# Optimization experiments

Measured on AMD Instinct MI355X. Metric: run time of the kernel, lower is better.

Reference implementation:

```python
import jax, jax.numpy as jnp
import numpy as np

B, S, D = 4, 2048, 1024
H, HD = 16, 64
WINDOW = 128


def setup_inputs() -> dict:
    key = jax.random.key(0)
    ks = jax.random.split(key, 8)
    scale = 1.0 / np.sqrt(D)
    return {
        "hidden_states": jax.random.normal(ks[0], (B, S, D), dtype=jnp.float32),
        "attention_mask": jnp.zeros((B, 1, 1, S), dtype=jnp.float32),
        "Wq": jax.random.normal(ks[1], (D, D), dtype=jnp.float32) * scale,
        "bq": jnp.zeros((D,), dtype=jnp.float32),
        "Wk": jax.random.normal(ks[2], (D, D), dtype=jnp.float32) * scale,
        "bk": jnp.zeros((D,), dtype=jnp.float32),
        "Wv": jax.random.normal(ks[3], (D, D), dtype=jnp.float32) * scale,
        "bv": jnp.zeros((D,), dtype=jnp.float32),
    }


def _proj(x, W, b):
    # [b t D] -> [b h t d]
    p = x @ W.T + b
    return p.reshape(x.shape[0], x.shape[1], H, HD).transpose(0, 2, 1, 3)


def reference(hidden_states, attention_mask, Wq, bq, Wk, bk, Wv, bv):
    q = _proj(hidden_states, Wq, bq)  # [b h t d]
    k = _proj(hidden_states, Wk, bk)
    v = _proj(hidden_states, Wv, bv)

    scores = jnp.einsum("bhtd,bhsd->bhts", q, k) / np.sqrt(HD)  # [b h t s]
    pos = jnp.arange(S)
    i, j = pos[:, None], pos[None, :]
    # causal (j <= i) AND sliding window (i - j <= w)
    allowed = (j <= i) & ((i - j) <= WINDOW)  # [t s]
    scores = jnp.where(allowed[None, None], scores, -jnp.inf)
    scores = scores + attention_mask  # additive padding mask [b,1,1,s]
    probs = jax.nn.softmax(scores, axis=-1)  # dropout identity in eval
    ctx = jnp.einsum("bhts,bhsd->bhtd", probs, v)
    return ctx.transpose(0, 2, 1, 3).reshape(B, S, D)
```

## Files before the change

kernel.cpp:

```cpp
#include <hip/hip_runtime.h>
#include <cstdint>

#define BDIM 4
#define SEQ 2048
#define DMODEL 1024
#define NH 16
#define HDIM 64

typedef __attribute__((ext_vector_type(8))) short bf16x8;
typedef __attribute__((ext_vector_type(4))) float f32x4;
typedef __attribute__((ext_vector_type(4))) int i32x4;
typedef __attribute__((ext_vector_type(4))) unsigned short u16x4;

#define MFMA16(a, b, c) __builtin_amdgcn_mfma_f32_16x16x32_bf16(a, b, c, 0, 0, 0)

__device__ __forceinline__ unsigned short f2bf(float x) {
    unsigned int u = __float_as_uint(x);
    unsigned int r = (u + 0x7FFFu + ((u >> 16) & 1u)) >> 16;
    return (unsigned short)r;
}

__device__ __forceinline__ void gload16(const void* g, void* l) {
    __builtin_amdgcn_global_load_lds(
        (const __attribute__((address_space(1))) unsigned int*)g,
        (__attribute__((address_space(3))) unsigned int*)l, 16, 0, 0);
}

__global__ __launch_bounds__(256) void k_cvt_x(const float* __restrict__ src,
                                               unsigned short* __restrict__ dst) {
    int i = blockIdx.x * 256 + threadIdx.x;
    float4 v = ((const float4*)src)[i];
    u16x4 o = {f2bf(v.x), f2bf(v.y), f2bf(v.z), f2bf(v.w)};
    ((u16x4*)dst)[i] = o;
}

__global__ __launch_bounds__(256) void k_cvt_w(const float* __restrict__ wq,
                                               const float* __restrict__ wk,
                                               const float* __restrict__ wv,
                                               unsigned short* __restrict__ dst) {
    int i = blockIdx.x * 256 + threadIdx.x;
    int e = i << 2;
    int which = e >> 20;
    int off = e & 0xFFFFF;
    const float* s = which == 0 ? wq : (which == 1 ? wk : wv);
    float4 v = *(const float4*)(s + off);
    u16x4 o = {f2bf(v.x), f2bf(v.y), f2bf(v.z), f2bf(v.w)};
    ((u16x4*)dst)[i] = o;
}

__global__ __launch_bounds__(256) __attribute__((amdgpu_waves_per_eu(4)))
void k_qkv(const unsigned short* __restrict__ X,
           const unsigned short* __restrict__ W,
           const float* __restrict__ bq,
           const float* __restrict__ bk,
           const float* __restrict__ bv,
           unsigned short* __restrict__ Qo,
           unsigned short* __restrict__ Ko,
           unsigned short* __restrict__ Vt) {
    __shared__ unsigned short ldsA[128 * 64];
    __shared__ unsigned short ldsB[128 * 64];
    const int tid = threadIdx.x;
    const int lane = tid & 63, wid = tid >> 6;
    const int wm = wid >> 1, wn = wid & 1;
    const int l15 = lane & 15, g = lane >> 4;
    const int m0 = blockIdx.y * 128, n0 = blockIdx.x * 128;

    f32x4 acc[4][4];
#pragma unroll
    for (int i = 0; i < 4; ++i)
#pragma unroll
        for (int j = 0; j < 4; ++j) acc[i][j] = (f32x4){0.f, 0.f, 0.f, 0.f};

    for (int kt = 0; kt < 16; ++kt) {
        const int k0 = kt << 6;
        __syncthreads();
#pragma unroll
        for (int it = 0; it < 4; ++it) {
            const int c = it * 256 + tid;
            const int row = c >> 3, sl = c & 7;
            const int slx = sl ^ (row & 7);
            gload16(X + (size_t)(m0 + row) * DMODEL + k0 + slx * 8, (char*)ldsA + c * 16);
            gload16(W + (size_t)(n0 + row) * DMODEL + k0 + slx * 8, (char*)ldsB + c * 16);
        }
        __syncthreads();
#pragma unroll
        for (int kk = 0; kk < 2; ++kk) {
            bf16x8 a[4], b[4];
#pragma unroll
            for (int f = 0; f < 4; ++f) {
                const int ra = wm * 64 + f * 16 + l15;
                a[f] = *(const bf16x8*)((const char*)ldsA +
                        ((ra * 128 + kk * 64 + g * 16) ^ ((ra & 7) << 4)));
                const int rb = wn * 64 + f * 16 + l15;
                b[f] = *(const bf16x8*)((const char*)ldsB +
                        ((rb * 128 + kk * 64 + g * 16) ^ ((rb & 7) << 4)));
            }
#pragma unroll
            for (int fm = 0; fm < 4; ++fm)
#pragma unroll
                for (int fn = 0; fn < 4; ++fn) acc[fm][fn] = MFMA16(a[fm], b[fn], acc[fm][fn]);
        }
    }

    const int bb = m0 >> 11;
    const int sbase = (m0 & 2047) + wm * 64 + g * 4;
#pragma unroll
    for (int fn = 0; fn < 4; ++fn) {
        const int col = n0 + wn * 64 + fn * 16 + l15;
        const int proj = col >> 10, rem = col & 1023;
        const int h = rem >> 6, hd = rem & 63;
        const float bias = (proj == 0 ? bq : proj == 1 ? bk : bv)[rem];
        const float scl = (proj == 0) ? 0.125f : 1.0f;
        unsigned short* dstp = (proj == 0 ? Qo : proj == 1 ? Ko : Vt) +
                               (size_t)(bb * NH + h) * (SEQ * HDIM) +
                               (proj == 2 ? (size_t)hd * SEQ : (size_t)hd);
        const int stride = (proj == 2) ? 1 : HDIM;
#pragma unroll
        for (int fm = 0; fm < 4; ++fm) {
            const int s0 = sbase + fm * 16;
#pragma unroll
            for (int r = 0; r < 4; ++r)
                dstp[(size_t)(s0 + r) * stride] = f2bf((acc[fm][fn][r] + bias) * scl);
        }
    }
}

__global__ __launch_bounds__(256) void k_attn(const unsigned short* __restrict__ Qg,
                                              const unsigned short* __restrict__ Kg,
                                              const unsigned short* __restrict__ Vtg,
                                              const float* __restrict__ amask,
                                              float* __restrict__ out) {
    __shared__ unsigned short kl[224 * 64];
    __shared__ unsigned short vl[64 * 224];
    __shared__ unsigned short pl[4 * 16 * 160];
    const int bid0 = blockIdx.x;
    const int bid = (bid0 & 7) * 256 + (bid0 >> 3);
    const int bh = bid >> 5, qb = bid & 31;
    const int b = bh >> 4, h = bh & 15;
    const int q0 = qb << 6;
    const int kstart = q0 - 144;
    const int tid = threadIdx.x, lane = tid & 63, w = tid >> 6;
    const int l15 = lane & 15, g = lane >> 4;

#pragma unroll
    for (int it = 0; it < 7; ++it) {
        const int c = it * 256 + tid;
        {
            const int row = c >> 3, sl = c & 7;
            const int key = kstart + row;
            i32x4 v = {0, 0, 0, 0};
            if ((unsigned)key < (unsigned)SEQ)
                v = *(const i32x4*)(Kg + (size_t)(bh * SEQ + key) * HDIM + sl * 8);
            *(i32x4*)((char*)kl + ((row * 128 + sl * 16) ^ ((row & 7) << 4))) = v;
        }
        {
            const int row = c / 28, sl = c - row * 28;
            const int key0 = kstart + sl * 8;
            i32x4 v = {0, 0, 0, 0};
            if ((unsigned)key0 < (unsigned)SEQ)
                v = *(const i32x4*)(Vtg + (size_t)(bh * HDIM + row) * SEQ + key0);
            *(i32x4*)((char*)vl + ((row * 448 + sl * 16) ^ ((row & 7) << 4))) = v;
        }
    }
    const int iq = q0 + w * 16 + l15;
    const bf16x8 qf0 = *(const bf16x8*)(Qg + (size_t)(bh * SEQ + iq) * HDIM + g * 8);
    const bf16x8 qf1 = *(const bf16x8*)(Qg + (size_t)(bh * SEQ + iq) * HDIM + 32 + g * 8);
    __syncthreads();

    char* pbase = (char*)pl + w * 5120;
    const int swq = (l15 & 7) << 4;
    float s[40];

    __builtin_amdgcn_s_setprio(1);
#pragma unroll
    for (int t = 0; t < 5; ++t) {
        const int tloc = w * 16 + t * 32;
        bf16x8 kf[2][2];
#pragma unroll
        for (int m = 0; m < 2; ++m) {
            const int row = tloc + m * 16 + l15;
            const int swz = (row & 7) << 4;
            kf[m][0] = *(const bf16x8*)((const char*)kl + ((row * 128 + g * 16) ^ swz));
            kf[m][1] = *(const bf16x8*)((const char*)kl + ((row * 128 + 64 + g * 16) ^ swz));
        }
        f32x4 sa0 = {0.f, 0.f, 0.f, 0.f}, sa1 = {0.f, 0.f, 0.f, 0.f};
        sa0 = MFMA16(kf[0][0], qf0, sa0);
        sa0 = MFMA16(kf[0][1], qf1, sa0);
        sa1 = MFMA16(kf[1][0], qf0, sa1);
        sa1 = MFMA16(kf[1][1], qf1, sa1);
#pragma unroll
        for (int f = 0; f < 2; ++f) {
            const int jb = kstart + tloc + f * 16 + g * 4;
            float4 m4 = {0.f, 0.f, 0.f, 0.f};
            if ((unsigned)jb < (unsigned)SEQ) m4 = *(const float4*)(amask + b * SEQ + jb);
            const float mvv[4] = {m4.x, m4.y, m4.z, m4.w};
#pragma unroll
            for (int r = 0; r < 4; ++r) {
                const int jg = jb + r;
                const float sc = (f == 0 ? sa0[r] : sa1[r]) + mvv[r];
                const bool ok = (jg >= 0) && (jg <= iq) && (iq - jg <= 128);
                s[t * 8 + f * 4 + r] = ok ? sc : -3.0e38f;
            }
        }
    }
    __builtin_amdgcn_s_setprio(0);

    float tr[20];
#pragma unroll
    for (int i = 0; i < 20; ++i) tr[i] = fmaxf(s[i], s[i + 20]);
#pragma unroll
    for (int i = 0; i < 10; ++i) tr[i] = fmaxf(tr[i], tr[i + 10]);
#pragma unroll
    for (int i = 0; i < 5; ++i) tr[i] = fmaxf(tr[i], tr[i + 5]);
    float m = fmaxf(fmaxf(tr[0], tr[1]), fmaxf(tr[2], fmaxf(tr[3], tr[4])));
    m = fmaxf(m, __shfl_xor(m, 16));
    m = fmaxf(m, __shfl_xor(m, 32));

    float ls0 = 0.f, ls1 = 0.f, ls2 = 0.f, ls3 = 0.f;
#pragma unroll
    for (int i = 0; i < 40; i += 4) {
        float p0 = exp2f((s[i + 0] - m) * 1.44269504f);
        float p1 = exp2f((s[i + 1] - m) * 1.44269504f);
        float p2 = exp2f((s[i + 2] - m) * 1.44269504f);
        float p3 = exp2f((s[i + 3] - m) * 1.44269504f);
        s[i + 0] = p0; s[i + 1] = p1; s[i + 2] = p2; s[i + 3] = p3;
        ls0 += p0; ls1 += p1; ls2 += p2; ls3 += p3;
    }
    float l = (ls0 + ls1) + (ls2 + ls3);
    l += __shfl_xor(l, 16);
    l += __shfl_xor(l, 32);

#pragma unroll
    for (int t = 0; t < 5; ++t) {
#pragma unroll
        for (int f = 0; f < 2; ++f) {
            u16x4 pu = {f2bf(s[t * 8 + f * 4 + 0]), f2bf(s[t * 8 + f * 4 + 1]),
                        f2bf(s[t * 8 + f * 4 + 2]), f2bf(s[t * 8 + f * 4 + 3])};
            *(u16x4*)(pbase + ((l15 * 320 + t * 64 + f * 32 + g * 8) ^ swq)) = pu;
        }
    }
    asm volatile("s_waitcnt lgkmcnt(0)" ::: "memory");
    __builtin_amdgcn_sched_barrier(0);

    f32x4 acc[4];
#pragma unroll
    for (int i = 0; i < 4; ++i) acc[i] = (f32x4){0.f, 0.f, 0.f, 0.f};
    __builtin_amdgcn_s_setprio(1);
#pragma unroll
    for (int t = 0; t < 5; ++t) {
        const int tloc = w * 16 + t * 32;
        const bf16x8 pf = *(const bf16x8*)(pbase + ((l15 * 320 + t * 64 + g * 16) ^ swq));
#pragma unroll
        for (int fn = 0; fn < 4; ++fn) {
            const int vrow = fn * 16 + l15;
            const bf16x8 vf = *(const bf16x8*)((const char*)vl +
                ((vrow * 448 + tloc * 2 + g * 16) ^ ((vrow & 7) << 4)));
            acc[fn] = MFMA16(pf, vf, acc[fn]);
        }
    }
    __builtin_amdgcn_s_setprio(0);

    float linv[4];
#pragma unroll
    for (int r = 0; r < 4; ++r) linv[r] = 1.0f / __shfl(l, g * 4 + r);
#pragma unroll
    for (int fn = 0; fn < 4; ++fn) {
#pragma unroll
        for (int r = 0; r < 4; ++r) {
            const int qrow = q0 + w * 16 + g * 4 + r;
            out[(size_t)(b * SEQ + qrow) * DMODEL + h * HDIM + fn * 16 + l15] =
                acc[fn][r] * linv[r];
        }
    }
}

extern "C" void kernel_launch(void* const* d_in, const int* in_sizes, int n_in,
                              void* d_out, int out_size, void* d_ws, size_t ws_size,
                              hipStream_t stream) {
    const float* hs = (const float*)d_in[0];
    const float* amask = (const float*)d_in[1];
    const float* wq = (const float*)d_in[2];
    const float* bq = (const float*)d_in[3];
    const float* wk = (const float*)d_in[4];
    const float* bk = (const float*)d_in[5];
    const float* wv = (const float*)d_in[6];
    const float* bv = (const float*)d_in[7];
    float* out = (float*)d_out;

    char* p = (char*)d_ws;
    unsigned short* Xbf = (unsigned short*)p;
    unsigned short* Wbf = (unsigned short*)(p + 16777216);
    unsigned short* Vtb = (unsigned short*)(p + 16777216 + 6291456);
    unsigned short* Qb = Vtb + 8388608;
    unsigned short* Kb = Qb + 8388608;

    k_cvt_x<<<8192, 256, 0, stream>>>(hs, Xbf);
    k_cvt_w<<<3072, 256, 0, stream>>>(wq, wk, wv, Wbf);
    k_qkv<<<dim3(24, 64), 256, 0, stream>>>(Xbf, Wbf, bq, bk, bv, Qb, Kb, Vtb);
    k_attn<<<2048, 256, 0, stream>>>(Qb, Kb, Vtb, amask, out);
}
```

Measured before the change: 138.2 us.

## Rewrite QKV GEMM as 256x256 tile with double-buffered async LDS pipeline

The QKV projection GEMM moves from 128x128 tiles with 256 threads to 256x256 tiles with 512 threads (8 waves, each owning 128x64). LDS is double-buffered in K-halves so global-to-LDS loads for later K steps overlap the MFMA work, with explicit vmcnt waits, barriers and s_setprio. The aim is more data reuse per tile and hidden load latency. The costs are only 384 blocks (fewer than before, with possible wave quantization on the CU count), more accumulator registers, and the loss of the XOR swizzle on LDS, which may bring back bank conflicts.

New measurement: 154.3 us. 11.6% more time.

```diff
diff --git a/kernel.cpp b/kernel.cpp
--- a/kernel.cpp
+++ b/kernel.cpp
@@ -48,7 +48,7 @@
     ((u16x4*)dst)[i] = o;
 }
 
-__global__ __launch_bounds__(256) __attribute__((amdgpu_waves_per_eu(4)))
+__global__ __launch_bounds__(512, 2)
 void k_qkv(const unsigned short* __restrict__ X,
            const unsigned short* __restrict__ W,
            const float* __restrict__ bq,
@@ -57,56 +57,137 @@
            unsigned short* __restrict__ Qo,
            unsigned short* __restrict__ Ko,
            unsigned short* __restrict__ Vt) {
-    __shared__ unsigned short ldsA[128 * 64];
-    __shared__ unsigned short ldsB[128 * 64];
+    __shared__ unsigned short ldsA[2][2][256 * 32];
+    __shared__ unsigned short ldsB[2][2][256 * 32];
     const int tid = threadIdx.x;
     const int lane = tid & 63, wid = tid >> 6;
-    const int wm = wid >> 1, wn = wid & 1;
+    const int wm = wid >> 2, wn = wid & 3;
     const int l15 = lane & 15, g = lane >> 4;
-    const int m0 = blockIdx.y * 128, n0 = blockIdx.x * 128;
-
-    f32x4 acc[4][4];
-#pragma unroll
-    for (int i = 0; i < 4; ++i)
+    const int m0 = blockIdx.y * 256, n0 = blockIdx.x * 256;
+
+#define STAGE_A(c, kk, kt)                                                        \
+    {                                                                             \
+        _Pragma("unroll") for (int i = 0; i < 2; ++i) {                           \
+            const int e = i * 512 + tid;                                          \
+            const int row = e >> 2, cc = e & 3;                                   \
+            gload16(X + (size_t)(m0 + row) * DMODEL + (kt)*64 + (kk)*32 + cc * 8, \
+                    (char*)&ldsA[c][kk][0] + e * 16);                             \
+        }                                                                         \
+    }
+#define STAGE_B(c, kk, kt)                                                        \
+    {                                                                             \
+        _Pragma("unroll") for (int i = 0; i < 2; ++i) {                           \
+            const int e = i * 512 + tid;                                          \
+            const int row = e >> 2, cc = e & 3;                                   \
+            gload16(W + (size_t)(n0 + row) * DMODEL + (kt)*64 + (kk)*32 + cc * 8, \
+                    (char*)&ldsB[c][kk][0] + e * 16);                             \
+        }                                                                         \
+    }
+
+    f32x4 acc[8][4];
+#pragma unroll
+    for (int i = 0; i < 8; ++i)
 #pragma unroll
         for (int j = 0; j < 4; ++j) acc[i][j] = (f32x4){0.f, 0.f, 0.f, 0.f};
 
-    for (int kt = 0; kt < 16; ++kt) {
-        const int k0 = kt << 6;
-        __syncthreads();
-#pragma unroll
-        for (int it = 0; it < 4; ++it) {
-            const int c = it * 256 + tid;
-            const int row = c >> 3, sl = c & 7;
-            const int slx = sl ^ (row & 7);
-            gload16(X + (size_t)(m0 + row) * DMODEL + k0 + slx * 8, (char*)ldsA + c * 16);
-            gload16(W + (size_t)(n0 + row) * DMODEL + k0 + slx * 8, (char*)ldsB + c * 16);
-        }
-        __syncthreads();
-#pragma unroll
-        for (int kk = 0; kk < 2; ++kk) {
-            bf16x8 a[4], b[4];
-#pragma unroll
-            for (int f = 0; f < 4; ++f) {
-                const int ra = wm * 64 + f * 16 + l15;
-                a[f] = *(const bf16x8*)((const char*)ldsA +
-                        ((ra * 128 + kk * 64 + g * 16) ^ ((ra & 7) << 4)));
-                const int rb = wn * 64 + f * 16 + l15;
-                b[f] = *(const bf16x8*)((const char*)ldsB +
-                        ((rb * 128 + kk * 64 + g * 16) ^ ((rb & 7) << 4)));
-            }
-#pragma unroll
-            for (int fm = 0; fm < 4; ++fm)
-#pragma unroll
-                for (int fn = 0; fn < 4; ++fn) acc[fm][fn] = MFMA16(a[fm], b[fn], acc[fm][fn]);
+    STAGE_A(0, 0, 0); STAGE_B(0, 0, 0);
+    STAGE_A(0, 1, 0); STAGE_B(0, 1, 0);
+    STAGE_A(1, 0, 1); STAGE_B(1, 0, 1);
+    asm volatile("s_waitcnt vmcnt(8)" ::: "memory");
+    __builtin_amdgcn_s_barrier();
+
+    const int arow = wm * 128 + l15;
+    const int brow = wn * 64 + l15;
+
+    for (int t = 0; t < 16; ++t) {
+        const int c = t & 1;
+        const char* Ab0 = (const char*)&ldsA[c][0][0];
+        const char* Ab1 = (const char*)&ldsA[c][1][0];
+        const char* Bb0 = (const char*)&ldsB[c][0][0];
+        const char* Bb1 = (const char*)&ldsB[c][1][0];
+
+        {
+            bf16x8 av[8], bv0, bv1;
+#pragma unroll
+            for (int mf = 0; mf < 8; ++mf)
+                av[mf] = *(const bf16x8*)(Ab0 + (arow + mf * 16) * 64 + g * 16);
+            bv0 = *(const bf16x8*)(Bb0 + (brow) * 64 + g * 16);
+            bv1 = *(const bf16x8*)(Bb0 + (brow + 16) * 64 + g * 16);
+            if (t < 15) STAGE_A(c ^ 1, 1, t + 1);
+            __builtin_amdgcn_s_barrier();
+            asm volatile("s_waitcnt lgkmcnt(0)" ::: "memory");
+            __builtin_amdgcn_sched_barrier(0);
+            __builtin_amdgcn_s_setprio(1);
+#pragma unroll
+            for (int mf = 0; mf < 8; ++mf) {
+                acc[mf][0] = MFMA16(av[mf], bv0, acc[mf][0]);
+                acc[mf][1] = MFMA16(av[mf], bv1, acc[mf][1]);
+            }
+            __builtin_amdgcn_s_setprio(0);
+            __builtin_amdgcn_s_barrier();
+
+            bv0 = *(const bf16x8*)(Bb0 + (brow + 32) * 64 + g * 16);
+            bv1 = *(const bf16x8*)(Bb0 + (brow + 48) * 64 + g * 16);
+            if (t < 15) STAGE_B(c ^ 1, 1, t + 1);
+            __builtin_amdgcn_s_barrier();
+            asm volatile("s_waitcnt lgkmcnt(0)" ::: "memory");
+            __builtin_amdgcn_sched_barrier(0);
+            __builtin_amdgcn_s_setprio(1);
+#pragma unroll
+            for (int mf = 0; mf < 8; ++mf) {
+                acc[mf][2] = MFMA16(av[mf], bv0, acc[mf][2]);
+                acc[mf][3] = MFMA16(av[mf], bv1, acc[mf][3]);
+            }
+            __builtin_amdgcn_s_setprio(0);
+            if (t < 15) { asm volatile("s_waitcnt vmcnt(8)" ::: "memory"); }
+            else        { asm volatile("s_waitcnt vmcnt(0)" ::: "memory"); }
+            __builtin_amdgcn_s_barrier();
+        }
+
+        {
+            bf16x8 av[8], bv0, bv1;
+#pragma unroll
+            for (int mf = 0; mf < 8; ++mf)
+                av[mf] = *(const bf16x8*)(Ab1 + (arow + mf * 16) * 64 + g * 16);
+            bv0 = *(const bf16x8*)(Bb1 + (brow) * 64 + g * 16);
+            bv1 = *(const bf16x8*)(Bb1 + (brow + 16) * 64 + g * 16);
+            if (t < 14) STAGE_A(c, 0, t + 2);
+            __builtin_amdgcn_s_barrier();
+            asm volatile("s_waitcnt lgkmcnt(0)" ::: "memory");
+            __builtin_amdgcn_sched_barrier(0);
+            __builtin_amdgcn_s_setprio(1);
+#pragma unroll
+            for (int mf = 0; mf < 8; ++mf) {
+                acc[mf][0] = MFMA16(av[mf], bv0, acc[mf][0]);
+                acc[mf][1] = MFMA16(av[mf], bv1, acc[mf][1]);
+            }
+            __builtin_amdgcn_s_setprio(0);
+            __builtin_amdgcn_s_barrier();
+
+            bv0 = *(const bf16x8*)(Bb1 + (brow + 32) * 64 + g * 16);
+            bv1 = *(const bf16x8*)(Bb1 + (brow + 48) * 64 + g * 16);
+            if (t < 14) STAGE_B(c, 0, t + 2);
+            __builtin_amdgcn_s_barrier();
+            asm volatile("s_waitcnt lgkmcnt(0)" ::: "memory");
+            __builtin_amdgcn_sched_barrier(0);
+            __builtin_amdgcn_s_setprio(1);
+#pragma unroll
+            for (int mf = 0; mf < 8; ++mf) {
+                acc[mf][2] = MFMA16(av[mf], bv0, acc[mf][2]);
+                acc[mf][3] = MFMA16(av[mf], bv1, acc[mf][3]);
+            }
+            __builtin_amdgcn_s_setprio(0);
+            if (t < 14)      { asm volatile("s_waitcnt vmcnt(8)" ::: "memory"); }
+            else if (t == 14){ asm volatile("s_waitcnt vmcnt(4)" ::: "memory"); }
+            __builtin_amdgcn_s_barrier();
         }
     }
 
     const int bb = m0 >> 11;
-    const int sbase = (m0 & 2047) + wm * 64 + g * 4;
-#pragma unroll
-    for (int fn = 0; fn < 4; ++fn) {
-        const int col = n0 + wn * 64 + fn * 16 + l15;
+    const int sbase = (m0 & 2047) + wm * 128 + g * 4;
+#pragma unroll
+    for (int nf = 0; nf < 4; ++nf) {
+        const int col = n0 + wn * 64 + nf * 16 + l15;
         const int proj = col >> 10, rem = col & 1023;
         const int h = rem >> 6, hd = rem & 63;
         const float bias = (proj == 0 ? bq : proj == 1 ? bk : bv)[rem];
@@ -116,13 +197,15 @@
                                (proj == 2 ? (size_t)hd * SEQ : (size_t)hd);
         const int stride = (proj == 2) ? 1 : HDIM;
 #pragma unroll
-        for (int fm = 0; fm < 4; ++fm) {
-            const int s0 = sbase + fm * 16;
+        for (int mf = 0; mf < 8; ++mf) {
+            const int s0 = sbase + mf * 16;
 #pragma unroll
             for (int r = 0; r < 4; ++r)
-                dstp[(size_t)(s0 + r) * stride] = f2bf((acc[fm][fn][r] + bias) * scl);
-        }
-    }
+                dstp[(size_t)(s0 + r) * stride] = f2bf((acc[mf][nf][r] + bias) * scl);
+        }
+    }
+#undef STAGE_A
+#undef STAGE_B
 }
 
 __global__ __launch_bounds__(256) void k_attn(const unsigned short* __restrict__ Qg,
@@ -296,6 +379,6 @@
 
     k_cvt_x<<<8192, 256, 0, stream>>>(hs, Xbf);
     k_cvt_w<<<3072, 256, 0, stream>>>(wq, wk, wv, Wbf);
-    k_qkv<<<dim3(24, 64), 256, 0, stream>>>(Xbf, Wbf, bq, bk, bv, Qb, Kb, Vtb);
+    k_qkv<<<dim3(12, 32), 512, 0, stream>>>(Xbf, Wbf, bq, bk, bv, Qb, Kb, Vtb);
     k_attn<<<2048, 256, 0, stream>>>(Qb, Kb, Vtb, amask, out);
 }
```

## Restructure QKV GEMM into 4-stage pipelined 256x128 tiles with 512 threads

Applied to the files above, without the earlier changes.

The QKV projection GEMM now uses 512-thread blocks, each computing a 256x128 output tile with K-slices of 32 held in a 4-deep LDS ring buffer. Global-to-LDS loads for slice t+3 are issued while slice t is computed, with explicit vmcnt waits and a single barrier per iteration in place of the previous two syncs per 64-wide K step. The grid is flattened to 768 blocks with an XCD-aware block remap, and MFMA sections are given raised wave priority. This is meant to hide global load latency and improve L2 reuse, at the cost of larger LDS use and hand-tuned waitcnt logic that must match the exact load count.

Result: slower. 141.3 us (+2.2%).

```diff
diff --git a/kernel.cpp b/kernel.cpp
--- a/kernel.cpp
+++ b/kernel.cpp
@@ -48,7 +48,7 @@
     ((u16x4*)dst)[i] = o;
 }
 
-__global__ __launch_bounds__(256) __attribute__((amdgpu_waves_per_eu(4)))
+__global__ __launch_bounds__(512, 2)
 void k_qkv(const unsigned short* __restrict__ X,
            const unsigned short* __restrict__ W,
            const float* __restrict__ bq,
@@ -57,13 +57,35 @@
            unsigned short* __restrict__ Qo,
            unsigned short* __restrict__ Ko,
            unsigned short* __restrict__ Vt) {
-    __shared__ unsigned short ldsA[128 * 64];
-    __shared__ unsigned short ldsB[128 * 64];
+    __shared__ unsigned short ldsA[4][256 * 32];
+    __shared__ unsigned short ldsB[4][128 * 32];
     const int tid = threadIdx.x;
     const int lane = tid & 63, wid = tid >> 6;
     const int wm = wid >> 1, wn = wid & 1;
     const int l15 = lane & 15, g = lane >> 4;
-    const int m0 = blockIdx.y * 128, n0 = blockIdx.x * 128;
+    const int bid0 = blockIdx.x;
+    const int bid = (bid0 & 7) * 96 + (bid0 >> 3);
+    const int bx = bid % 24, by = bid / 24;
+    const int m0 = by * 256, n0 = bx * 128;
+
+#define STAGE_A(d, kt)                                                      \
+    {                                                                       \
+        _Pragma("unroll") for (int i = 0; i < 2; ++i) {                     \
+            const int e = i * 512 + tid;                                    \
+            const int row = e >> 2, sl = e & 3;                             \
+            const int slx = sl ^ ((row >> 1) & 3);                          \
+            gload16(X + (size_t)(m0 + row) * DMODEL + (kt) * 32 + slx * 8,  \
+                    (char*)&ldsA[d][0] + e * 16);                           \
+        }                                                                   \
+    }
+#define STAGE_B(d, kt)                                                      \
+    {                                                                       \
+        const int e = tid;                                                  \
+        const int row = e >> 2, sl = e & 3;                                 \
+        const int slx = sl ^ ((row >> 1) & 3);                              \
+        gload16(W + (size_t)(n0 + row) * DMODEL + (kt) * 32 + slx * 8,      \
+                (char*)&ldsB[d][0] + e * 16);                               \
+    }
 
     f32x4 acc[4][4];
 #pragma unroll
@@ -71,42 +93,54 @@
 #pragma unroll
         for (int j = 0; j < 4; ++j) acc[i][j] = (f32x4){0.f, 0.f, 0.f, 0.f};
 
-    for (int kt = 0; kt < 16; ++kt) {
-        const int k0 = kt << 6;
-        __syncthreads();
-#pragma unroll
-        for (int it = 0; it < 4; ++it) {
-            const int c = it * 256 + tid;
-            const int row = c >> 3, sl = c & 7;
-            const int slx = sl ^ (row & 7);
-            gload16(X + (size_t)(m0 + row) * DMODEL + k0 + slx * 8, (char*)ldsA + c * 16);
-            gload16(W + (size_t)(n0 + row) * DMODEL + k0 + slx * 8, (char*)ldsB + c * 16);
-        }
-        __syncthreads();
-#pragma unroll
-        for (int kk = 0; kk < 2; ++kk) {
-            bf16x8 a[4], b[4];
-#pragma unroll
-            for (int f = 0; f < 4; ++f) {
-                const int ra = wm * 64 + f * 16 + l15;
-                a[f] = *(const bf16x8*)((const char*)ldsA +
-                        ((ra * 128 + kk * 64 + g * 16) ^ ((ra & 7) << 4)));
-                const int rb = wn * 64 + f * 16 + l15;
-                b[f] = *(const bf16x8*)((const char*)ldsB +
-                        ((rb * 128 + kk * 64 + g * 16) ^ ((rb & 7) << 4)));
-            }
-#pragma unroll
-            for (int fm = 0; fm < 4; ++fm)
-#pragma unroll
-                for (int fn = 0; fn < 4; ++fn) acc[fm][fn] = MFMA16(a[fm], b[fn], acc[fm][fn]);
-        }
-    }
+    STAGE_A(0, 0); STAGE_B(0, 0);
+    STAGE_A(1, 1); STAGE_B(1, 1);
+    STAGE_A(2, 2); STAGE_B(2, 2);
+    asm volatile("s_waitcnt vmcnt(6)" ::: "memory");
+    __builtin_amdgcn_s_barrier();
+
+    const int ar = wm * 64 + l15;
+    const int br = wn * 64 + l15;
+
+#pragma unroll 4
+    for (int t = 0; t < 32; ++t) {
+        const int cb = t & 3;
+        bf16x8 av[4], bvv[4];
+#pragma unroll
+        for (int mf = 0; mf < 4; ++mf) {
+            const int row = ar + mf * 16;
+            av[mf] = *(const bf16x8*)((const char*)&ldsA[cb][0] +
+                      ((row * 64 + g * 16) ^ (((row >> 1) & 3) << 4)));
+        }
+#pragma unroll
+        for (int nf = 0; nf < 4; ++nf) {
+            const int row = br + nf * 16;
+            bvv[nf] = *(const bf16x8*)((const char*)&ldsB[cb][0] +
+                       ((row * 64 + g * 16) ^ (((row >> 1) & 3) << 4)));
+        }
+        if (t < 29) { STAGE_A((t + 3) & 3, t + 3); STAGE_B((t + 3) & 3, t + 3); }
+        asm volatile("s_waitcnt lgkmcnt(0)" ::: "memory");
+        __builtin_amdgcn_sched_barrier(0);
+        __builtin_amdgcn_s_setprio(1);
+#pragma unroll
+        for (int mf = 0; mf < 4; ++mf)
+#pragma unroll
+            for (int nf = 0; nf < 4; ++nf)
+                acc[mf][nf] = MFMA16(av[mf], bvv[nf], acc[mf][nf]);
+        __builtin_amdgcn_s_setprio(0);
+        if (t < 29)      { asm volatile("s_waitcnt vmcnt(6)" ::: "memory"); }
+        else if (t == 29){ asm volatile("s_waitcnt vmcnt(3)" ::: "memory"); }
+        else if (t == 30){ asm volatile("s_waitcnt vmcnt(0)" ::: "memory"); }
+        __builtin_amdgcn_s_barrier();
+    }
+#undef STAGE_A
+#undef STAGE_B
 
     const int bb = m0 >> 11;
     const int sbase = (m0 & 2047) + wm * 64 + g * 4;
 #pragma unroll
-    for (int fn = 0; fn < 4; ++fn) {
-        const int col = n0 + wn * 64 + fn * 16 + l15;
+    for (int nf = 0; nf < 4; ++nf) {
+        const int col = n0 + wn * 64 + nf * 16 + l15;
         const int proj = col >> 10, rem = col & 1023;
         const int h = rem >> 6, hd = rem & 63;
         const float bias = (proj == 0 ? bq : proj == 1 ? bk : bv)[rem];
@@ -116,11 +150,11 @@
                                (proj == 2 ? (size_t)hd * SEQ : (size_t)hd);
         const int stride = (proj == 2) ? 1 : HDIM;
 #pragma unroll
-        for (int fm = 0; fm < 4; ++fm) {
-            const int s0 = sbase + fm * 16;
+        for (int mf = 0; mf < 4; ++mf) {
+            const int s0 = sbase + mf * 16;
 #pragma unroll
             for (int r = 0; r < 4; ++r)
-                dstp[(size_t)(s0 + r) * stride] = f2bf((acc[fm][fn][r] + bias) * scl);
+                dstp[(size_t)(s0 + r) * stride] = f2bf((acc[mf][nf][r] + bias) * scl);
         }
     }
 }
@@ -296,6 +330,6 @@
 
     k_cvt_x<<<8192, 256, 0, stream>>>(hs, Xbf);
     k_cvt_w<<<3072, 256, 0, stream>>>(wq, wk, wv, Wbf);
-    k_qkv<<<dim3(24, 64), 256, 0, stream>>>(Xbf, Wbf, bq, bk, bv, Qb, Kb, Vtb);
+    k_qkv<<<768, 512, 0, stream>>>(Xbf, Wbf, bq, bk, bv, Qb, Kb, Vtb);
     k_attn<<<2048, 256, 0, stream>>>(Qb, Kb, Vtb, amask, out);
 }
```
